# Optimization experiments

Hardware: AMD Instinct MI355X
Metric: run time of the kernel (lower is better)

Reference implementation:

```python
import jax, jax.numpy as jnp
import numpy as np

B, N, D = 4096, 8192, 512
MARGIN = 1.0


def setup_inputs() -> dict:
    key = jax.random.key(0)
    k1, k2, k3 = jax.random.split(key, 3)
    anchor = jax.random.normal(k1, (B, D), dtype=jnp.float32)
    sample = jax.random.normal(k2, (N, D), dtype=jnp.float32)
    # L2-normalize: the module uses 1 - dot as a cosine-style distance
    anchor = anchor / jnp.linalg.norm(anchor, axis=1, keepdims=True)
    sample = sample / jnp.linalg.norm(sample, axis=1, keepdims=True)
    # one-hot positive label per anchor row (docstring: one-hot LongTensor)
    pos_pos = jax.random.randint(k3, (B,), 0, N)
    positive_idx = jax.nn.one_hot(pos_pos, N, dtype=jnp.int64)
    return {"anchor_features": anchor, "sample_features": sample,
            "positive_idx": positive_idx}


def reference(anchor_features, sample_features, positive_idx):
    # distances: [B, N]
    dist = 1.0 - jnp.matmul(anchor_features, sample_features.T)
    pos_mask = positive_idx.astype(bool)
    # exactly one positive per row -> pos_dist: [B]
    pos_dist = jnp.sum(jnp.where(pos_mask, dist, 0.0), axis=1)
    # hinge against every negative (num_neg=0, smooth=False branch)
    hinge = jnp.maximum(pos_dist[:, None] - dist + MARGIN, 0.0)  # [B, N]
    per_row = jnp.sum(jnp.where(pos_mask, 0.0, hinge), axis=1) / (N - 1)
    # losses summed over batch, then averaged (average=True)
    return jnp.mean(per_row)
```

## Files before the change

### kernel.cpp

```cpp
#include <hip/hip_runtime.h>
#include <hip/hip_bf16.h>
#include <stdint.h>

#define M_ROWS 4096
#define N_COLS 8192
#define KDIM   512

#define BM 256
#define BN 256
#define BKT 32
#define NKT (KDIM / BKT)
#define GTHREADS 512

typedef __attribute__((ext_vector_type(8))) __bf16 bf16x8;
typedef __attribute__((ext_vector_type(4))) float  f32x4;

#define BAR() do { asm volatile("" ::: "memory"); \
                   __builtin_amdgcn_s_barrier();  \
                   asm volatile("" ::: "memory"); } while (0)

__device__ __forceinline__ unsigned short f2bf(float f) {
  union { float f; uint32_t u; } v; v.f = f;
  uint32_t u = v.u;
  u += 0x7fffu + ((u >> 16) & 1u);
  return (unsigned short)(u >> 16);
}

__global__ void prep_kernel(const float* __restrict__ A,
                            const float* __restrict__ S,
                            const int* __restrict__ onehot,
                            float* __restrict__ s_pos,
                            unsigned short* __restrict__ Abf,
                            unsigned short* __restrict__ Sbf) {
  const int b = blockIdx.x;
  const int tid = threadIdx.x;

  #pragma unroll
  for (int i = 0; i < 2; ++i) {
    int li = tid + i * 256;
    if (li < 384) {
      int idx = b * 384 + li;
      float4 v; ushort4 o;
      if (idx < 524288) {
        v = reinterpret_cast<const float4*>(A)[idx];
        o.x = f2bf(v.x); o.y = f2bf(v.y); o.z = f2bf(v.z); o.w = f2bf(v.w);
        reinterpret_cast<ushort4*>(Abf)[idx] = o;
      } else {
        int k = idx - 524288;
        v = reinterpret_cast<const float4*>(S)[k];
        o.x = f2bf(v.x); o.y = f2bf(v.y); o.z = f2bf(v.z); o.w = f2bf(v.w);
        reinterpret_cast<ushort4*>(Sbf)[k] = o;
      }
    }
  }

  __shared__ int pos_s;
  if (tid == 0) pos_s = 0;
  __syncthreads();
  const int4* row = reinterpret_cast<const int4*>(onehot + (size_t)b * N_COLS);
  for (int i = tid; i < N_COLS / 4; i += 256) {
    int4 v = row[i];
    if (v.x | v.y | v.z | v.w) {
      int j = i * 4 + (v.x ? 0 : (v.y ? 1 : (v.z ? 2 : 3)));
      pos_s = j;
    }
  }
  __syncthreads();
  const int j = pos_s;

  float sum = 0.f;
  const float* a = A + (size_t)b * KDIM;
  const float* s = S + (size_t)j * KDIM;
  for (int d = tid; d < KDIM; d += 256) sum += a[d] * s[d];
  #pragma unroll
  for (int off = 32; off > 0; off >>= 1) sum += __shfl_down(sum, off, 64);
  __shared__ float wsum[4];
  const int wid = tid >> 6, lane = tid & 63;
  if (lane == 0) wsum[wid] = sum;
  __syncthreads();
  if (tid == 0) s_pos[b] = (wsum[0] + wsum[1]) + (wsum[2] + wsum[3]);
}

__device__ __forceinline__ int swz_x(int r) { return (r & 3) ^ ((r >> 2) & 3); }

__device__ __forceinline__ bf16x8 lds_frag(const unsigned short* chunk, int r, int lk) {
  int g = lk ^ swz_x(r);
  return *reinterpret_cast<const bf16x8*>(chunk + r * 32 + g * 8);
}

__device__ __forceinline__ void stage_chunk(const unsigned short* __restrict__ srcBase,
                                            int tt, unsigned short* chunk,
                                            int w, int l) {
  #pragma unroll
  for (int jj = 0; jj < 2; ++jj) {
    int r = jj * 128 + w * 16 + (l >> 2);
    int g = (l & 3) ^ swz_x(r);
    const unsigned short* src = srcBase + (size_t)r * KDIM + tt * BKT + g * 8;
    __builtin_amdgcn_global_load_lds(
        (const __attribute__((address_space(1))) void*)src,
        (__attribute__((address_space(3))) void*)(chunk + jj * 4096 + w * 512),
        16, 0, 0);
  }
}

template<bool STAGE, int VM>
__device__ __forceinline__ void ktile(int t, unsigned short (*lds)[2][BM * BKT],
                                      const unsigned short* __restrict__ Abase,
                                      const unsigned short* __restrict__ Sbase,
                                      f32x4 (&acc)[8][4],
                                      int wr, int wc, int lr, int lk, int w, int l) {
  const unsigned short* cA = lds[t & 3][0];
  const unsigned short* cB = lds[t & 3][1];
  bf16x8 bfr[4], afr[4];
  #pragma unroll
  for (int n = 0; n < 4; ++n) bfr[n] = lds_frag(cB, wc * 64 + n * 16 + lr, lk);
  #pragma unroll
  for (int m = 0; m < 4; ++m) afr[m] = lds_frag(cA, wr * 128 + m * 16 + lr, lk);
  if (STAGE) stage_chunk(Abase, t + 3, lds[(t + 3) & 3][0], w, l);
  BAR();
  __builtin_amdgcn_s_setprio(1);
  #pragma unroll
  for (int m = 0; m < 4; ++m)
    #pragma unroll
    for (int n = 0; n < 4; ++n)
      acc[m][n] = __builtin_amdgcn_mfma_f32_16x16x32_bf16(afr[m], bfr[n],
                                                          acc[m][n], 0, 0, 0);
  __builtin_amdgcn_s_setprio(0);
  BAR();
  #pragma unroll
  for (int m = 0; m < 4; ++m) afr[m] = lds_frag(cA, wr * 128 + (m + 4) * 16 + lr, lk);
  if (STAGE) stage_chunk(Sbase, t + 3, lds[(t + 3) & 3][1], w, l);
  BAR();
  __builtin_amdgcn_s_setprio(1);
  #pragma unroll
  for (int m = 0; m < 4; ++m)
    #pragma unroll
    for (int n = 0; n < 4; ++n)
      acc[m + 4][n] = __builtin_amdgcn_mfma_f32_16x16x32_bf16(afr[m], bfr[n],
                                                              acc[m + 4][n], 0, 0, 0);
  __builtin_amdgcn_s_setprio(0);
  if (VM == 8)      asm volatile("s_waitcnt vmcnt(8)" ::: "memory");
  else if (VM == 4) asm volatile("s_waitcnt vmcnt(4)" ::: "memory");
  else if (VM == 0) asm volatile("s_waitcnt vmcnt(0)" ::: "memory");
  BAR();
}

__global__ __launch_bounds__(GTHREADS, 2) void gemm_hinge_kernel(
    const unsigned short* __restrict__ Abf,
    const unsigned short* __restrict__ Sbf,
    const float* __restrict__ s_pos,
    double* __restrict__ partial) {
  __shared__ alignas(16) unsigned short lds[4][2][BM * BKT];
  __shared__ float wred[8];

  const int t    = threadIdx.x;
  const int w    = t >> 6;
  const int lane = t & 63;
  const int wr   = w >> 2;
  const int wc   = w & 3;
  const int lr   = lane & 15;
  const int lk   = lane >> 4;
  const int bx   = blockIdx.x;
  const int rowBase = (bx & 15) * BM;
  const int colBase = (bx >> 4) * BN;

  const unsigned short* Abase = Abf + (size_t)rowBase * KDIM;
  const unsigned short* Sbase = Sbf + (size_t)colBase * KDIM;

  f32x4 acc[8][4];
  #pragma unroll
  for (int m = 0; m < 8; ++m)
    #pragma unroll
    for (int n = 0; n < 4; ++n)
      acc[m][n] = (f32x4){0.f, 0.f, 0.f, 0.f};

  #pragma unroll
  for (int tt = 0; tt < 3; ++tt) {
    stage_chunk(Abase, tt, lds[tt][0], w, lane);
    stage_chunk(Sbase, tt, lds[tt][1], w, lane);
  }
  asm volatile("s_waitcnt vmcnt(8)" ::: "memory");
  BAR();

  #pragma unroll 1
  for (int kt = 0; kt < NKT - 3; ++kt)
    ktile<true, 8>(kt, lds, Abase, Sbase, acc, wr, wc, lr, lk, w, lane);
  ktile<false, 4>(NKT - 3, lds, Abase, Sbase, acc, wr, wc, lr, lk, w, lane);
  ktile<false, 0>(NKT - 2, lds, Abase, Sbase, acc, wr, wc, lr, lk, w, lane);
  ktile<false, -1>(NKT - 1, lds, Abase, Sbase, acc, wr, wc, lr, lk, w, lane);

  float lsum = 0.f;
  const int rl = lk * 4;
  #pragma unroll
  for (int m = 0; m < 8; ++m) {
    float sp[4];
    #pragma unroll
    for (int r = 0; r < 4; ++r)
      sp[r] = s_pos[rowBase + wr * 128 + m * 16 + rl + r];
    #pragma unroll
    for (int n = 0; n < 4; ++n)
      #pragma unroll
      for (int r = 0; r < 4; ++r)
        lsum += fmaxf(acc[m][n][r] - sp[r] + 1.0f, 0.f);
  }
  #pragma unroll
  for (int off = 32; off > 0; off >>= 1) lsum += __shfl_down(lsum, off, 64);
  if (lane == 0) wred[w] = lsum;
  __syncthreads();
  if (t == 0) {
    float s = 0.f;
    #pragma unroll
    for (int i = 0; i < 8; ++i) s += wred[i];
    partial[bx] = (double)s;
  }
}

__global__ void finalize_kernel(const double* __restrict__ partial,
                                float* __restrict__ out) {
  __shared__ double sdata[256];
  double s = 0.0;
  for (int i = threadIdx.x; i < 512; i += 256) s += partial[i];
  sdata[threadIdx.x] = s;
  __syncthreads();
  for (int st = 128; st > 0; st >>= 1) {
    if (threadIdx.x < st) sdata[threadIdx.x] += sdata[threadIdx.x + st];
    __syncthreads();
  }
  if (threadIdx.x == 0) {
    double v = (sdata[0] - (double)M_ROWS) / ((double)M_ROWS * (double)(N_COLS - 1));
    *out = (float)v;
  }
}

extern "C" void kernel_launch(void* const* d_in, const int* in_sizes, int n_in,
                              void* d_out, int out_size, void* d_ws, size_t ws_size,
                              hipStream_t stream) {
  const float* A  = (const float*)d_in[0];
  const float* S  = (const float*)d_in[1];
  const int*   oh = (const int*)d_in[2];
  float* out = (float*)d_out;

  char* ws = (char*)d_ws;
  double* partial = (double*)ws;
  float* s_pos    = (float*)(ws + 16384);
  unsigned short* Abf = (unsigned short*)(ws + 32768);
  unsigned short* Sbf = Abf + (size_t)M_ROWS * KDIM;

  prep_kernel<<<M_ROWS, 256, 0, stream>>>(A, S, oh, s_pos, Abf, Sbf);
  gemm_hinge_kernel<<<512, GTHREADS, 0, stream>>>(Abf, Sbf, s_pos, partial);
  finalize_kernel<<<1, 256, 0, stream>>>(partial, out);
}
```

Before: 70.18 us.

## Fuse one-hot scan into GEMM and defer hinge via per-row sum/min

Moves the one-hot label scan (128MB of int data) out of the prep kernel and streams it with nontemporal loads inside the GEMM k-loop, so it overlaps with MFMA work. The GEMM epilogue no longer needs the positive distance. It emits per-row partial sums and minima instead, and a new finalize kernel computes the exact positive dot in fp32. It applies the hinge algebraically when every dot clears the threshold, and falls back to a slow exact recompute otherwise. This adds extra workspace traffic for the partials and a very slow path if the min check fails.

Measured after the change: 103.1 us. 1.47x slower.

```diff
diff --git a/kernel.cpp b/kernel.cpp
--- a/kernel.cpp
+++ b/kernel.cpp
@@ -9,11 +9,11 @@
 #define BM 256
 #define BN 256
 #define BKT 32
-#define NKT (KDIM / BKT)
-#define GTHREADS 512
+#define NKT 16
 
 typedef __attribute__((ext_vector_type(8))) __bf16 bf16x8;
 typedef __attribute__((ext_vector_type(4))) float  f32x4;
+typedef __attribute__((ext_vector_type(4))) int    i32x4;
 
 #define BAR() do { asm volatile("" ::: "memory"); \
                    __builtin_amdgcn_s_barrier();  \
@@ -26,59 +26,26 @@
   return (unsigned short)(u >> 16);
 }
 
-__global__ void prep_kernel(const float* __restrict__ A,
-                            const float* __restrict__ S,
-                            const int* __restrict__ onehot,
-                            float* __restrict__ s_pos,
-                            unsigned short* __restrict__ Abf,
-                            unsigned short* __restrict__ Sbf) {
-  const int b = blockIdx.x;
-  const int tid = threadIdx.x;
-
-  #pragma unroll
-  for (int i = 0; i < 2; ++i) {
-    int li = tid + i * 256;
-    if (li < 384) {
-      int idx = b * 384 + li;
-      float4 v; ushort4 o;
-      if (idx < 524288) {
-        v = reinterpret_cast<const float4*>(A)[idx];
-        o.x = f2bf(v.x); o.y = f2bf(v.y); o.z = f2bf(v.z); o.w = f2bf(v.w);
-        reinterpret_cast<ushort4*>(Abf)[idx] = o;
-      } else {
-        int k = idx - 524288;
-        v = reinterpret_cast<const float4*>(S)[k];
-        o.x = f2bf(v.x); o.y = f2bf(v.y); o.z = f2bf(v.z); o.w = f2bf(v.w);
-        reinterpret_cast<ushort4*>(Sbf)[k] = o;
-      }
-    }
-  }
-
-  __shared__ int pos_s;
-  if (tid == 0) pos_s = 0;
-  __syncthreads();
-  const int4* row = reinterpret_cast<const int4*>(onehot + (size_t)b * N_COLS);
-  for (int i = tid; i < N_COLS / 4; i += 256) {
-    int4 v = row[i];
-    if (v.x | v.y | v.z | v.w) {
-      int j = i * 4 + (v.x ? 0 : (v.y ? 1 : (v.z ? 2 : 3)));
-      pos_s = j;
-    }
-  }
-  __syncthreads();
-  const int j = pos_s;
-
-  float sum = 0.f;
-  const float* a = A + (size_t)b * KDIM;
-  const float* s = S + (size_t)j * KDIM;
-  for (int d = tid; d < KDIM; d += 256) sum += a[d] * s[d];
-  #pragma unroll
-  for (int off = 32; off > 0; off >>= 1) sum += __shfl_down(sum, off, 64);
-  __shared__ float wsum[4];
-  const int wid = tid >> 6, lane = tid & 63;
-  if (lane == 0) wsum[wid] = sum;
-  __syncthreads();
-  if (tid == 0) s_pos[b] = (wsum[0] + wsum[1]) + (wsum[2] + wsum[3]);
+__global__ __launch_bounds__(256) void cvt_kernel(const float* __restrict__ A,
+                                                  const float* __restrict__ S,
+                                                  unsigned short* __restrict__ Abf,
+                                                  unsigned short* __restrict__ Sbf) {
+  int g = blockIdx.x * 256 + threadIdx.x;
+  #pragma unroll
+  for (int it = 0; it < 4; ++it) {
+    int idx = g + it * 393216;
+    float4 v; ushort4 o;
+    if (idx < 524288) {
+      v = reinterpret_cast<const float4*>(A)[idx];
+      o.x = f2bf(v.x); o.y = f2bf(v.y); o.z = f2bf(v.z); o.w = f2bf(v.w);
+      reinterpret_cast<ushort4*>(Abf)[idx] = o;
+    } else {
+      int q = idx - 524288;
+      v = reinterpret_cast<const float4*>(S)[q];
+      o.x = f2bf(v.x); o.y = f2bf(v.y); o.z = f2bf(v.z); o.w = f2bf(v.w);
+      reinterpret_cast<ushort4*>(Sbf)[q] = o;
+    }
+  }
 }
 
 __device__ __forceinline__ int swz_x(int r) { return (r & 3) ^ ((r >> 2) & 3); }
@@ -103,20 +70,43 @@
   }
 }
 
-template<bool STAGE, int VM>
-__device__ __forceinline__ void ktile(int t, unsigned short (*lds)[2][BM * BKT],
-                                      const unsigned short* __restrict__ Abase,
-                                      const unsigned short* __restrict__ Sbase,
-                                      f32x4 (&acc)[8][4],
-                                      int wr, int wc, int lr, int lk, int w, int l) {
-  const unsigned short* cA = lds[t & 3][0];
-  const unsigned short* cB = lds[t & 3][1];
+template<int TSRC>
+__device__ __forceinline__ void consume_scan(i32x4 (&sv)[2][2], int* pos_lds, int tid) {
+  #pragma unroll
+  for (int j = 0; j < 2; ++j) {
+    i32x4 v = sv[TSRC & 1][j];
+    if (v[0] | v[1] | v[2] | v[3]) {
+      int li4 = (TSRC * 512 + tid) * 2 + j;
+      int sub = v[0] ? 0 : (v[1] ? 1 : (v[2] ? 2 : 3));
+      pos_lds[li4 >> 11] = ((li4 & 2047) << 2) + sub;
+    }
+  }
+}
+
+template<int T>
+__device__ __forceinline__ void do_tile(unsigned short (*lds)[2][BM * BKT],
+                                        const unsigned short* __restrict__ Abase,
+                                        const unsigned short* __restrict__ Sbase,
+                                        const i32x4* __restrict__ scanB,
+                                        int* pos_lds,
+                                        i32x4 (&sv)[2][2], f32x4 (&acc)[8][4],
+                                        int wr, int wc, int lr, int lk,
+                                        int w, int lane, int tid) {
+  constexpr bool STAGE = (T <= NKT - 4);
+  const unsigned short* cA = lds[T & 3][0];
+  const unsigned short* cB = lds[T & 3][1];
+
+  if constexpr (T >= 2) consume_scan<T - 2>(sv, pos_lds, tid);
+
   bf16x8 bfr[4], afr[4];
   #pragma unroll
   for (int n = 0; n < 4; ++n) bfr[n] = lds_frag(cB, wc * 64 + n * 16 + lr, lk);
   #pragma unroll
   for (int m = 0; m < 4; ++m) afr[m] = lds_frag(cA, wr * 128 + m * 16 + lr, lk);
-  if (STAGE) stage_chunk(Abase, t + 3, lds[(t + 3) & 3][0], w, l);
+  if constexpr (STAGE) stage_chunk(Abase, T + 3, lds[(T + 3) & 3][0], w, lane);
+  #pragma unroll
+  for (int j = 0; j < 2; ++j)
+    sv[T & 1][j] = __builtin_nontemporal_load(scanB + (size_t)((T * 512 + tid) * 2 + j));
   BAR();
   __builtin_amdgcn_s_setprio(1);
   #pragma unroll
@@ -129,7 +119,7 @@
   BAR();
   #pragma unroll
   for (int m = 0; m < 4; ++m) afr[m] = lds_frag(cA, wr * 128 + (m + 4) * 16 + lr, lk);
-  if (STAGE) stage_chunk(Sbase, t + 3, lds[(t + 3) & 3][1], w, l);
+  if constexpr (STAGE) stage_chunk(Sbase, T + 3, lds[(T + 3) & 3][1], w, lane);
   BAR();
   __builtin_amdgcn_s_setprio(1);
   #pragma unroll
@@ -139,33 +129,34 @@
       acc[m + 4][n] = __builtin_amdgcn_mfma_f32_16x16x32_bf16(afr[m], bfr[n],
                                                               acc[m + 4][n], 0, 0, 0);
   __builtin_amdgcn_s_setprio(0);
-  if (VM == 8)      asm volatile("s_waitcnt vmcnt(8)" ::: "memory");
-  else if (VM == 4) asm volatile("s_waitcnt vmcnt(4)" ::: "memory");
-  else if (VM == 0) asm volatile("s_waitcnt vmcnt(0)" ::: "memory");
-  BAR();
-}
-
-__global__ __launch_bounds__(GTHREADS, 2) void gemm_hinge_kernel(
+  if constexpr (T == 0)                 asm volatile("s_waitcnt vmcnt(10)" ::: "memory");
+  else if constexpr (T >= 1 && T <= 12) asm volatile("s_waitcnt vmcnt(12)" ::: "memory");
+  else if constexpr (T == 13)           asm volatile("s_waitcnt vmcnt(8)"  ::: "memory");
+  else if constexpr (T == 14)           asm volatile("s_waitcnt vmcnt(4)"  ::: "memory");
+  BAR();
+}
+
+__global__ __launch_bounds__(512, 2) void gemm_scan_kernel(
     const unsigned short* __restrict__ Abf,
     const unsigned short* __restrict__ Sbf,
-    const float* __restrict__ s_pos,
-    double* __restrict__ partial) {
+    const int* __restrict__ onehot,
+    int* __restrict__ pos_idx,
+    float* __restrict__ rsum, float* __restrict__ rmin) {
   __shared__ alignas(16) unsigned short lds[4][2][BM * BKT];
-  __shared__ float wred[8];
-
-  const int t    = threadIdx.x;
-  const int w    = t >> 6;
-  const int lane = t & 63;
-  const int wr   = w >> 2;
-  const int wc   = w & 3;
-  const int lr   = lane & 15;
-  const int lk   = lane >> 4;
+  __shared__ int pos_lds[8];
+
+  const int tid  = threadIdx.x;
   const int bx   = blockIdx.x;
-  const int rowBase = (bx & 15) * BM;
-  const int colBase = (bx >> 4) * BN;
+  const int w    = tid >> 6;
+  const int lane = tid & 63;
+  const int wr   = w >> 2, wc = w & 3;
+  const int lr   = lane & 15, lk = lane >> 4;
+  const int rp   = bx & 15, cp = bx >> 4;
+  const int rowBase = rp * BM;
 
   const unsigned short* Abase = Abf + (size_t)rowBase * KDIM;
-  const unsigned short* Sbase = Sbf + (size_t)colBase * KDIM;
+  const unsigned short* Sbase = Sbf + (size_t)cp * BN * KDIM;
+  const i32x4* scanB = reinterpret_cast<const i32x4*>(onehot + (size_t)bx * 8 * N_COLS);
 
   f32x4 acc[8][4];
   #pragma unroll
@@ -173,6 +164,7 @@
     #pragma unroll
     for (int n = 0; n < 4; ++n)
       acc[m][n] = (f32x4){0.f, 0.f, 0.f, 0.f};
+  i32x4 sv[2][2];
 
   #pragma unroll
   for (int tt = 0; tt < 3; ++tt) {
@@ -182,54 +174,124 @@
   asm volatile("s_waitcnt vmcnt(8)" ::: "memory");
   BAR();
 
-  #pragma unroll 1
-  for (int kt = 0; kt < NKT - 3; ++kt)
-    ktile<true, 8>(kt, lds, Abase, Sbase, acc, wr, wc, lr, lk, w, lane);
-  ktile<false, 4>(NKT - 3, lds, Abase, Sbase, acc, wr, wc, lr, lk, w, lane);
-  ktile<false, 0>(NKT - 2, lds, Abase, Sbase, acc, wr, wc, lr, lk, w, lane);
-  ktile<false, -1>(NKT - 1, lds, Abase, Sbase, acc, wr, wc, lr, lk, w, lane);
-
-  float lsum = 0.f;
-  const int rl = lk * 4;
-  #pragma unroll
-  for (int m = 0; m < 8; ++m) {
-    float sp[4];
-    #pragma unroll
-    for (int r = 0; r < 4; ++r)
-      sp[r] = s_pos[rowBase + wr * 128 + m * 16 + rl + r];
-    #pragma unroll
-    for (int n = 0; n < 4; ++n)
+  do_tile<0>(lds, Abase, Sbase, scanB, pos_lds, sv, acc, wr, wc, lr, lk, w, lane, tid);
+  do_tile<1>(lds, Abase, Sbase, scanB, pos_lds, sv, acc, wr, wc, lr, lk, w, lane, tid);
+  do_tile<2>(lds, Abase, Sbase, scanB, pos_lds, sv, acc, wr, wc, lr, lk, w, lane, tid);
+  do_tile<3>(lds, Abase, Sbase, scanB, pos_lds, sv, acc, wr, wc, lr, lk, w, lane, tid);
+  do_tile<4>(lds, Abase, Sbase, scanB, pos_lds, sv, acc, wr, wc, lr, lk, w, lane, tid);
+  do_tile<5>(lds, Abase, Sbase, scanB, pos_lds, sv, acc, wr, wc, lr, lk, w, lane, tid);
+  do_tile<6>(lds, Abase, Sbase, scanB, pos_lds, sv, acc, wr, wc, lr, lk, w, lane, tid);
+  do_tile<7>(lds, Abase, Sbase, scanB, pos_lds, sv, acc, wr, wc, lr, lk, w, lane, tid);
+  do_tile<8>(lds, Abase, Sbase, scanB, pos_lds, sv, acc, wr, wc, lr, lk, w, lane, tid);
+  do_tile<9>(lds, Abase, Sbase, scanB, pos_lds, sv, acc, wr, wc, lr, lk, w, lane, tid);
+  do_tile<10>(lds, Abase, Sbase, scanB, pos_lds, sv, acc, wr, wc, lr, lk, w, lane, tid);
+  do_tile<11>(lds, Abase, Sbase, scanB, pos_lds, sv, acc, wr, wc, lr, lk, w, lane, tid);
+  do_tile<12>(lds, Abase, Sbase, scanB, pos_lds, sv, acc, wr, wc, lr, lk, w, lane, tid);
+  do_tile<13>(lds, Abase, Sbase, scanB, pos_lds, sv, acc, wr, wc, lr, lk, w, lane, tid);
+  do_tile<14>(lds, Abase, Sbase, scanB, pos_lds, sv, acc, wr, wc, lr, lk, w, lane, tid);
+  do_tile<15>(lds, Abase, Sbase, scanB, pos_lds, sv, acc, wr, wc, lr, lk, w, lane, tid);
+
+  consume_scan<14>(sv, pos_lds, tid);
+  consume_scan<15>(sv, pos_lds, tid);
+  __syncthreads();
+
+  float* eps = (float*)&lds[0][0][0];
+  float* epm = eps + 4096;
+  #pragma unroll
+  for (int m = 0; m < 8; ++m)
+    #pragma unroll
+    for (int r = 0; r < 4; ++r) {
+      float s_ = (acc[m][0][r] + acc[m][1][r]) + (acc[m][2][r] + acc[m][3][r]);
+      float n_ = fminf(fminf(acc[m][0][r], acc[m][1][r]),
+                       fminf(acc[m][2][r], acc[m][3][r]));
+      s_ += __shfl_xor(s_, 4, 64);
+      n_ = fminf(n_, __shfl_xor(n_, 4, 64));
+      s_ += __shfl_xor(s_, 8, 64);
+      n_ = fminf(n_, __shfl_xor(n_, 8, 64));
+      if ((lane & 12) == 0) {
+        int row = wr * 128 + m * 16 + lk * 4 + r;
+        int cls = lane & 3;
+        eps[(row * 4 + cls) * 4 + wc] = s_;
+        epm[(row * 4 + cls) * 4 + wc] = n_;
+      }
+    }
+  __syncthreads();
+  #pragma unroll
+  for (int item = tid; item < 1024; item += 512) {
+    int row = item >> 2, cls = item & 3;
+    float s0 = (eps[item * 4 + 0] + eps[item * 4 + 1]) +
+               (eps[item * 4 + 2] + eps[item * 4 + 3]);
+    float m0 = fminf(fminf(epm[item * 4 + 0], epm[item * 4 + 1]),
+                     fminf(epm[item * 4 + 2], epm[item * 4 + 3]));
+    size_t gi = (size_t)(rowBase + row) * 128 + cp * 4 + cls;
+    rsum[gi] = s0;
+    rmin[gi] = m0;
+  }
+  if (tid < 8) pos_idx[bx * 8 + tid] = pos_lds[tid];
+}
+
+__global__ __launch_bounds__(256) void fin1_kernel(
+    const float* __restrict__ A, const float* __restrict__ Sm,
+    const int* __restrict__ pos_idx,
+    const float* __restrict__ rsum, const float* __restrict__ rmin,
+    float* __restrict__ rowLoss) {
+  const int w = threadIdx.x >> 6, lane = threadIdx.x & 63;
+  #pragma unroll
+  for (int i = 0; i < 2; ++i) {
+    int row = blockIdx.x * 8 + w * 2 + i;
+    int j = pos_idx[row];
+    const float4* a4 = reinterpret_cast<const float4*>(A + (size_t)row * KDIM);
+    const float4* s4 = reinterpret_cast<const float4*>(Sm + (size_t)j * KDIM);
+    float4 x0 = a4[lane * 2], x1 = a4[lane * 2 + 1];
+    float4 y0 = s4[lane * 2], y1 = s4[lane * 2 + 1];
+    float dp = x0.x * y0.x + x0.y * y0.y + x0.z * y0.z + x0.w * y0.w
+             + x1.x * y1.x + x1.y * y1.y + x1.z * y1.z + x1.w * y1.w;
+    float rs = rsum[(size_t)row * 128 + lane] + rsum[(size_t)row * 128 + 64 + lane];
+    float rm = fminf(rmin[(size_t)row * 128 + lane],
+                     rmin[(size_t)row * 128 + 64 + lane]);
+    #pragma unroll
+    for (int off = 32; off > 0; off >>= 1) {
+      dp += __shfl_down(dp, off, 64);
+      rs += __shfl_down(rs, off, 64);
+      rm = fminf(rm, __shfl_down(rm, off, 64));
+    }
+    float p  = __shfl(dp, 0, 64);
+    float R  = __shfl(rs, 0, 64);
+    float mn = __shfl(rm, 0, 64);
+    float loss;
+    if (mn >= p - 1.0f) {
+      loss = (R - p) - (float)(N_COLS - 1) * (p - 1.0f);
+    } else {
+      float accv = 0.f;
+      const float* arow = A + (size_t)row * KDIM;
+      for (int n = lane; n < N_COLS; n += 64) {
+        const float* srow = Sm + (size_t)n * KDIM;
+        float d = 0.f;
+        for (int k = 0; k < KDIM; ++k) d += arow[k] * srow[k];
+        float h = fmaxf(d - p + 1.0f, 0.0f);
+        accv += (n == j) ? 0.f : h;
+      }
       #pragma unroll
-      for (int r = 0; r < 4; ++r)
-        lsum += fmaxf(acc[m][n][r] - sp[r] + 1.0f, 0.f);
-  }
-  #pragma unroll
-  for (int off = 32; off > 0; off >>= 1) lsum += __shfl_down(lsum, off, 64);
-  if (lane == 0) wred[w] = lsum;
-  __syncthreads();
-  if (t == 0) {
-    float s = 0.f;
-    #pragma unroll
-    for (int i = 0; i < 8; ++i) s += wred[i];
-    partial[bx] = (double)s;
-  }
-}
-
-__global__ void finalize_kernel(const double* __restrict__ partial,
-                                float* __restrict__ out) {
-  __shared__ double sdata[256];
+      for (int off = 32; off > 0; off >>= 1) accv += __shfl_down(accv, off, 64);
+      loss = __shfl(accv, 0, 64);
+    }
+    if (lane == 0) rowLoss[row] = loss;
+  }
+}
+
+__global__ __launch_bounds__(256) void fin2_kernel(const float* __restrict__ rowLoss,
+                                                   float* __restrict__ out) {
+  __shared__ double sd[256];
   double s = 0.0;
-  for (int i = threadIdx.x; i < 512; i += 256) s += partial[i];
-  sdata[threadIdx.x] = s;
+  for (int i = threadIdx.x; i < M_ROWS; i += 256) s += (double)rowLoss[i];
+  sd[threadIdx.x] = s;
   __syncthreads();
   for (int st = 128; st > 0; st >>= 1) {
-    if (threadIdx.x < st) sdata[threadIdx.x] += sdata[threadIdx.x + st];
+    if (threadIdx.x < st) sd[threadIdx.x] += sd[threadIdx.x + st];
     __syncthreads();
   }
-  if (threadIdx.x == 0) {
-    double v = (sdata[0] - (double)M_ROWS) / ((double)M_ROWS * (double)(N_COLS - 1));
-    *out = (float)v;
-  }
+  if (threadIdx.x == 0)
+    *out = (float)(sd[0] / ((double)M_ROWS * (double)(N_COLS - 1)));
 }
 
 extern "C" void kernel_launch(void* const* d_in, const int* in_sizes, int n_in,
@@ -241,12 +303,15 @@
   float* out = (float*)d_out;
 
   char* ws = (char*)d_ws;
-  double* partial = (double*)ws;
-  float* s_pos    = (float*)(ws + 16384);
-  unsigned short* Abf = (unsigned short*)(ws + 32768);
+  int*   pos_idx  = (int*)ws;
+  float* rsum     = (float*)(ws + 16384);
+  float* rmin     = (float*)(ws + 16384 + 2097152);
+  float* rowLoss  = (float*)(ws + 16384 + 4194304);
+  unsigned short* Abf = (unsigned short*)(ws + 16384 + 4194304 + 16384);
   unsigned short* Sbf = Abf + (size_t)M_ROWS * KDIM;
 
-  prep_kernel<<<M_ROWS, 256, 0, stream>>>(A, S, oh, s_pos, Abf, Sbf);
-  gemm_hinge_kernel<<<512, GTHREADS, 0, stream>>>(Abf, Sbf, s_pos, partial);
-  finalize_kernel<<<1, 256, 0, stream>>>(partial, out);
-}
+  cvt_kernel<<<1536, 256, 0, stream>>>(A, S, Abf, Sbf);
+  gemm_scan_kernel<<<512, 512, 0, stream>>>(Abf, Sbf, oh, pos_idx, rsum, rmin);
+  fin1_kernel<<<512, 256, 0, stream>>>(A, S, pos_idx, rsum, rmin, rowLoss);
+  fin2_kernel<<<1, 256, 0, stream>>>(rowLoss, out);
+}
```
